# Kernel tuning notes

Measured on AMD Instinct MI355X. Metric: run time of the kernel, lower is better.

Reference implementation:

```python
import jax, jax.numpy as jnp
import numpy as np

N_SEQ, SEQ_LEN, BATCH, IN, H, OUT = 32, 256, 16, 32, 256, 1


def setup_inputs() -> dict:
    key = jax.random.key(0)
    ks = jax.random.split(key, 12)
    s = 1.0 / np.sqrt(H)  # torch RNNCell default init scale
    f32 = jnp.float32
    return {
        "x": jax.random.normal(ks[0], (N_SEQ, SEQ_LEN, BATCH, IN), f32),
        "flags": jax.random.randint(ks[1], (N_SEQ,), 0, 2, dtype=jnp.int32),
        "W_ih1": jax.random.normal(ks[2], (2, 4 * H, IN), f32) * s,
        "W_hh1": jax.random.normal(ks[3], (2, 4 * H, H), f32) * s,
        "b_ih1": jax.random.normal(ks[4], (2, 4 * H), f32) * s,
        "b_hh1": jax.random.normal(ks[5], (2, 4 * H), f32) * s,
        "W_ih2": jax.random.normal(ks[6], (4 * H, H), f32) * s,
        "W_hh2": jax.random.normal(ks[7], (4 * H, H), f32) * s,
        "b_ih2": jax.random.normal(ks[8], (4 * H,), f32) * s,
        "b_hh2": jax.random.normal(ks[9], (4 * H,), f32) * s,
        "W_lin": jax.random.normal(ks[10], (OUT, H), f32) * s,
        "b_lin": jax.random.normal(ks[11], (OUT,), f32) * s,
    }


def _lstm_cell(xt, h, c, Wih, Whh, b):
    # torch LSTMCell: gates = x@Wih.T + h@Whh.T + b_ih + b_hh; chunks i,f,g,o
    gates = xt @ Wih.T + h @ Whh.T + b
    i, f, g, o = jnp.split(gates, 4, axis=-1)
    c = jax.nn.sigmoid(f) * c + jax.nn.sigmoid(i) * jnp.tanh(g)
    h = jax.nn.sigmoid(o) * jnp.tanh(c)
    return h, c


def reference(x, flags, W_ih1, W_hh1, b_ih1, b_hh1,
              W_ih2, W_hh2, b_ih2, b_hh2, W_lin, b_lin):
    # flags selects layer1 (on-paper, idx 0) vs layer1_air (idx 1) per sequence
    Wih_s = W_ih1[flags]              # [N_SEQ, 4H, IN]
    Whh_s = W_hh1[flags]              # [N_SEQ, 4H, H]
    b_s = (b_ih1 + b_hh1)[flags]      # [N_SEQ, 4H]

    h0 = jnp.zeros((BATCH, H), x.dtype)

    def run_seq(xs, Wih, Whh, b):
        # hidden resets to zero at the start of every sequence -> independent scans
        def step(carry, xt):
            h, c = _lstm_cell(xt, *carry, Wih, Whh, b)
            return (h, c), None
        (h, _), _ = jax.lax.scan(step, (h0, h0), xs)
        return h

    h1 = jax.vmap(run_seq)(x, Wih_s, Whh_s, b_s)  # [N_SEQ, BATCH, H]

    # layer2: sequential LSTM over per-sequence final hiddens (dropout=0 -> identity)
    b2 = b_ih2 + b_hh2

    def step2(carry, hin):
        h, c = _lstm_cell(hin, *carry, W_ih2, W_hh2, b2)
        return (h, c), None

    (h2, _), _ = jax.lax.scan(step2, (h0, h0), h1)
    return jax.nn.sigmoid(h2 @ W_lin.T + b_lin)  # [BATCH, OUT]
```

## Files before the change

### kernel.cpp

```cpp
#include <hip/hip_runtime.h>
#include <hip/hip_bf16.h>

#define NSEQ   32
#define SEQLEN 256
#define NB     16
#define NIN    32
#define NH     256
#define G4     1024

typedef __attribute__((ext_vector_type(8))) short bf16x8;
typedef __attribute__((ext_vector_type(4))) float f32x4;
typedef unsigned long long ull;

__device__ __forceinline__ unsigned short f2bf(float f) {
    union { float f; unsigned u; } v; v.f = f;
    unsigned u = v.u;
    return (unsigned short)((u + 0x7FFFu + ((u >> 16) & 1u)) >> 16);
}
__device__ __forceinline__ float bf2f(unsigned short u) {
    union { unsigned u; float f; } v; v.u = ((unsigned)u) << 16; return v.f;
}
__device__ __forceinline__ float sigf(float x) { return 1.0f / (1.0f + __expf(-x)); }
__device__ __forceinline__ float tanhfast(float x) { return 1.0f - 2.0f / (__expf(2.0f * x) + 1.0f); }

__global__ void pack_w1(const float* __restrict__ Wih, const float* __restrict__ Whh,
                        unsigned short* __restrict__ Bp) {
    int idx = blockIdx.x * blockDim.x + threadIdx.x;
    if (idx >= 2 * 64 * 9 * 64) return;
    int fl   = idx / (64 * 9 * 64);
    int rem  = idx % (64 * 9 * 64);
    int tile = rem / (9 * 64);
    int kk   = (rem / 64) % 9;
    int l    = rem & 63;
    int n    = tile * 16 + (l & 15);
    int k0   = kk * 32 + (l >> 4) * 8;
    unsigned short* dst = Bp + (size_t)idx * 8;
#pragma unroll
    for (int j = 0; j < 8; ++j) {
        int k = k0 + j;
        float v = (k < NH) ? Whh[((size_t)fl * G4 + n) * NH + k]
                           : Wih[((size_t)fl * G4 + n) * NIN + (k - NH)];
        dst[j] = f2bf(v);
    }
}

__global__ void pack_w2(const float* __restrict__ Wih, const float* __restrict__ Whh,
                        unsigned short* __restrict__ Bp) {
    int idx = blockIdx.x * blockDim.x + threadIdx.x;
    if (idx >= 64 * 16 * 64) return;
    int tile = idx / (16 * 64);
    int kk   = (idx / 64) % 16;
    int l    = idx & 63;
    int n    = tile * 16 + (l & 15);
    int k0   = kk * 32 + (l >> 4) * 8;
    unsigned short* dst = Bp + (size_t)idx * 8;
#pragma unroll
    for (int j = 0; j < 8; ++j) {
        int k = k0 + j;
        float v = (k < NH) ? Whh[(size_t)n * NH + k] : Wih[(size_t)n * NH + (k - NH)];
        dst[j] = f2bf(v);
    }
}

#define STRA 320
#define ASH_BYTES (NB * STRA * 2)

__device__ __forceinline__ unsigned aoff(int row, int col) {
    return (((unsigned)(row * STRA + col)) * 2u) ^ (((unsigned)row & 7u) << 4);
}

__global__ __launch_bounds__(1024) void lstm_layer1(
    const float* __restrict__ x, const int* __restrict__ flags,
    const float* __restrict__ bih, const float* __restrict__ bhh,
    const unsigned short* __restrict__ Bp_all,
    unsigned short* __restrict__ h1bf,
    unsigned* __restrict__ hxu)
{
    __shared__ __align__(16) unsigned char Ash[ASH_BYTES];
    __shared__ float gate[4][64][17];

    const int bid = blockIdx.x;
    const int s   = bid & 31;
    const int j   = bid >> 5;
    const int tid = threadIdx.x;
    const int w = tid >> 6, l = tid & 63, lr = l & 15, kg = l >> 4;
    const int g = w >> 2, cg = w & 3;
    const int fl = flags[s];
    const int tile = g * 16 + j * 4 + cg;
    const unsigned short* Bp = Bp_all + (size_t)fl * (64 * 9 * 64 * 8);

    bf16x8 wreg[9];
#pragma unroll
    for (int kk = 0; kk < 9; ++kk)
        wreg[kk] = *(const bf16x8*)(Bp + ((size_t)(tile * 9 + kk) * 64 + l) * 8);

    const int grow = tile * 16 + lr;
    const float bias = bih[fl * G4 + grow] + bhh[fl * G4 + grow];

    const int pb = tid >> 6, pc = tid & 63;
    const int o0 = (((j + 1) & 3) << 6) + pc;
    const int o1 = (((j + 2) & 3) << 6) + pc;
    const int o2 = (((j + 3) & 3) << 6) + pc;
    const int xb = tid >> 5, xk = tid & 31;
    float cst = 0.f;

    unsigned* hxseq = hxu + (size_t)s * (2 * NB * 256);

    for (int i = tid * 4; i < ASH_BYTES; i += 1024 * 4)
        *(unsigned*)(Ash + i) = 0u;
    __syncthreads();
    if (tid < NB * NIN)
        *(unsigned short*)(Ash + aoff(xb, NH + xk)) =
            f2bf(x[(((size_t)s * SEQLEN) * NB + xb) * NIN + xk]);
    __syncthreads();

    for (int t = 0; t < SEQLEN; ++t) {
        float xpre = 0.f;
        if (t + 1 < SEQLEN && tid < NB * NIN)
            xpre = x[(((size_t)s * SEQLEN + t + 1) * NB + xb) * NIN + xk];

        f32x4 acc = {bias, bias, bias, bias};
#pragma unroll
        for (int kk = 0; kk < 9; ++kk) {
            bf16x8 a = *(const bf16x8*)(Ash + aoff(lr, kk * 32 + kg * 8));
            acc = __builtin_amdgcn_mfma_f32_16x16x32_bf16(a, wreg[kk], acc, 0, 0, 0);
        }
#pragma unroll
        for (int r = 0; r < 4; ++r)
            gate[g][cg * 16 + lr][kg * 4 + r] = acc[r];
        __syncthreads();

        float ig = gate[0][pc][pb], fg = gate[1][pc][pb];
        float gg = gate[2][pc][pb], og = gate[3][pc][pb];
        float cn = sigf(fg) * cst + sigf(ig) * tanhfast(gg);
        cst = cn;
        float h = sigf(og) * tanhfast(cn);
        unsigned short hb = f2bf(h);
        *(unsigned short*)(Ash + aoff(pb, (j << 6) + pc)) = hb;

        if (t == SEQLEN - 1) {
            h1bf[((size_t)s * NB + pb) * NH + (j << 6) + pc] = hb;
        } else {
            const unsigned tg = (unsigned)(t + 1);
            unsigned* row = hxseq + ((((t + 1) & 1) * NB + pb) << 8);
            __hip_atomic_store(row + (j << 6) + pc, ((unsigned)hb << 16) | tg,
                               __ATOMIC_RELAXED, __HIP_MEMORY_SCOPE_AGENT);
            if (tid < NB * NIN)
                *(unsigned short*)(Ash + aoff(xb, NH + xk)) = f2bf(xpre);
            unsigned v0 = __hip_atomic_load(row + o0, __ATOMIC_RELAXED, __HIP_MEMORY_SCOPE_AGENT);
            unsigned v1 = __hip_atomic_load(row + o1, __ATOMIC_RELAXED, __HIP_MEMORY_SCOPE_AGENT);
            unsigned v2 = __hip_atomic_load(row + o2, __ATOMIC_RELAXED, __HIP_MEMORY_SCOPE_AGENT);
            while ((v0 & 0xFFFFu) != tg)
                v0 = __hip_atomic_load(row + o0, __ATOMIC_RELAXED, __HIP_MEMORY_SCOPE_AGENT);
            while ((v1 & 0xFFFFu) != tg)
                v1 = __hip_atomic_load(row + o1, __ATOMIC_RELAXED, __HIP_MEMORY_SCOPE_AGENT);
            while ((v2 & 0xFFFFu) != tg)
                v2 = __hip_atomic_load(row + o2, __ATOMIC_RELAXED, __HIP_MEMORY_SCOPE_AGENT);
            *(unsigned short*)(Ash + aoff(pb, o0)) = (unsigned short)(v0 >> 16);
            *(unsigned short*)(Ash + aoff(pb, o1)) = (unsigned short)(v1 >> 16);
            *(unsigned short*)(Ash + aoff(pb, o2)) = (unsigned short)(v2 >> 16);
            __syncthreads();
        }
    }
}

#define STRA2 520

__global__ __launch_bounds__(1024, 4) void lstm_layer2(
    const unsigned short* __restrict__ h1bf,
    const float* __restrict__ bih2, const float* __restrict__ bhh2,
    const unsigned short* __restrict__ Bp2,
    const float* __restrict__ Wlin, const float* __restrict__ blin,
    float* __restrict__ out,
    ull* __restrict__ hx2)
{
    const int j = blockIdx.x;

    __shared__ __align__(16) unsigned short A_sh[NB * STRA2];
    __shared__ float gate[4][64][17];
    __shared__ float red[NB * 16];

    const int tid = threadIdx.x;
    const int w = tid >> 6, l = tid & 63, lr = l & 15, kg = l >> 4;
    const int g = w >> 2, cg = w & 3;
    const int tile = g * 16 + j * 4 + cg;

    bf16x8 wreg[16];
#pragma unroll
    for (int kk = 0; kk < 16; ++kk)
        wreg[kk] = *(const bf16x8*)(Bp2 + ((size_t)(tile * 16 + kk) * 64 + l) * 8);

    const int grow = tile * 16 + lr;
    const float bias = bih2[grow] + bhh2[grow];
    const int pb = tid >> 6, pc = tid & 63;
    float cst = 0.f;
    const int rb = tid >> 6, rc4 = (tid & 63) * 4;

    for (int i = tid; i < NB * NH; i += 1024)
        A_sh[(i >> 8) * STRA2 + (i & 255)] = 0;
    *(ushort4*)&A_sh[rb * STRA2 + NH + rc4] = *(const ushort4*)&h1bf[(size_t)rb * NH + rc4];
    __syncthreads();

    for (int sq = 0; sq < NSEQ; ++sq) {
        ushort4 pre = {0, 0, 0, 0};
        if (sq + 1 < NSEQ)
            pre = *(const ushort4*)&h1bf[((size_t)(sq + 1) * NB + rb) * NH + rc4];

        f32x4 acc = {bias, bias, bias, bias};
#pragma unroll
        for (int kk = 0; kk < 16; ++kk) {
            bf16x8 a = *(const bf16x8*)&A_sh[lr * STRA2 + kk * 32 + kg * 8];
            acc = __builtin_amdgcn_mfma_f32_16x16x32_bf16(a, wreg[kk], acc, 0, 0, 0);
        }
#pragma unroll
        for (int r = 0; r < 4; ++r)
            gate[g][cg * 16 + lr][kg * 4 + r] = acc[r];
        __syncthreads();

        {
            float ig = gate[0][pc][pb], fg = gate[1][pc][pb];
            float gg = gate[2][pc][pb], og = gate[3][pc][pb];
            float cn = sigf(fg) * cst + sigf(ig) * tanhfast(gg);
            cst = cn;
            float h = sigf(og) * tanhfast(cn);
            unsigned hw = ((unsigned)f2bf(h) << 16) | (unsigned)(sq + 1);
            A_sh[pb * STRA2 + (j << 6) + pc] = (unsigned short)(hw >> 16);
            __hip_atomic_store((unsigned*)hx2 + ((((sq + 1) & 1) * NB + pb) << 8) + (j << 6) + pc,
                               hw, __ATOMIC_RELAXED, __HIP_MEMORY_SCOPE_AGENT);
        }
        if (sq + 1 < NSEQ)
            *(ushort4*)&A_sh[rb * STRA2 + NH + rc4] = pre;

        {
            const unsigned tg = (unsigned)(sq + 1);
            unsigned* row = (unsigned*)hx2 + ((((sq + 1) & 1) * NB + pb) << 8);
            const int q0 = (((j + 1) & 3) << 6) + pc;
            const int q1 = (((j + 2) & 3) << 6) + pc;
            const int q2 = (((j + 3) & 3) << 6) + pc;
            unsigned v0 = __hip_atomic_load(row + q0, __ATOMIC_RELAXED, __HIP_MEMORY_SCOPE_AGENT);
            unsigned v1 = __hip_atomic_load(row + q1, __ATOMIC_RELAXED, __HIP_MEMORY_SCOPE_AGENT);
            unsigned v2 = __hip_atomic_load(row + q2, __ATOMIC_RELAXED, __HIP_MEMORY_SCOPE_AGENT);
            while ((v0 & 0xFFFFu) != tg)
                v0 = __hip_atomic_load(row + q0, __ATOMIC_RELAXED, __HIP_MEMORY_SCOPE_AGENT);
            while ((v1 & 0xFFFFu) != tg)
                v1 = __hip_atomic_load(row + q1, __ATOMIC_RELAXED, __HIP_MEMORY_SCOPE_AGENT);
            while ((v2 & 0xFFFFu) != tg)
                v2 = __hip_atomic_load(row + q2, __ATOMIC_RELAXED, __HIP_MEMORY_SCOPE_AGENT);
            A_sh[pb * STRA2 + q0] = (unsigned short)(v0 >> 16);
            A_sh[pb * STRA2 + q1] = (unsigned short)(v1 >> 16);
            A_sh[pb * STRA2 + q2] = (unsigned short)(v2 >> 16);
        }
        __syncthreads();
    }

    if (j == 0) {
        if (tid < 256) {
            int b = tid >> 4, kc = tid & 15;
            float pacc = 0.f;
#pragma unroll
            for (int k = 0; k < 16; ++k)
                pacc += bf2f(A_sh[b * STRA2 + kc * 16 + k]) * Wlin[kc * 16 + k];
            red[b * 16 + kc] = pacc;
        }
        __syncthreads();
        if (tid < 16) {
            float ssum = blin[0];
#pragma unroll
            for (int kc = 0; kc < 16; ++kc) ssum += red[tid * 16 + kc];
            out[tid] = 1.0f / (1.0f + __expf(-ssum));
        }
    }
}

extern "C" void kernel_launch(void* const* d_in, const int* in_sizes, int n_in,
                              void* d_out, int out_size, void* d_ws, size_t ws_size,
                              hipStream_t stream) {
    const float* x    = (const float*)d_in[0];
    const int*   flg  = (const int*)d_in[1];
    const float* Wih1 = (const float*)d_in[2];
    const float* Whh1 = (const float*)d_in[3];
    const float* bih1 = (const float*)d_in[4];
    const float* bhh1 = (const float*)d_in[5];
    const float* Wih2 = (const float*)d_in[6];
    const float* Whh2 = (const float*)d_in[7];
    const float* bih2 = (const float*)d_in[8];
    const float* bhh2 = (const float*)d_in[9];
    const float* Wlin = (const float*)d_in[10];
    const float* blin = (const float*)d_in[11];
    float* out = (float*)d_out;

    unsigned short* ws   = (unsigned short*)d_ws;
    unsigned short* Bp1  = ws;
    unsigned short* Bp2  = Bp1 + 589824;
    unsigned short* h1bf = Bp2 + 524288;
    unsigned*       hxu1 = (unsigned*)(h1bf + 131072);
    ull*            hx2  = (ull*)(hxu1 + 262144);

    hipMemsetAsync(hxu1, 0, 262144 * 4 + 4096 * 8, stream);

    pack_w1<<<dim3(288), dim3(256), 0, stream>>>(Wih1, Whh1, Bp1);
    pack_w2<<<dim3(256), dim3(256), 0, stream>>>(Wih2, Whh2, Bp2);
    lstm_layer1<<<dim3(128), dim3(1024), 0, stream>>>(x, flg, bih1, bhh1, Bp1, h1bf, hxu1);
    lstm_layer2<<<dim3(4), dim3(1024), 0, stream>>>(h1bf, bih2, bhh2, Bp2, Wlin, blin, out, hx2);
}
```

Before: 677.2 us.

## Add fast-path plain-load polling with atomic fallback and split MFMA accumulators

Each step writes its hidden-state word to two exchange buffers: a plain-store fast buffer and the existing agent-scope atomic buffer. Peers first poll the fast buffer with volatile loads under a budget and drop permanently to the atomic path if that ever times out. The aim is to cut cross-block handoff latency in the recurrent loop, relying on the hardware making plain stores visible to other CUs. The MFMA chains are also split across two accumulators to shorten the dependency chain. Layer2 now launches 32 blocks with only every eighth one active, apparently to spread the four working blocks across different XCDs.

Result: faster. 625.9 us (-7.6%).

```diff
diff --git a/kernel.cpp b/kernel.cpp
--- a/kernel.cpp
+++ b/kernel.cpp
@@ -74,7 +74,8 @@
     const float* __restrict__ bih, const float* __restrict__ bhh,
     const unsigned short* __restrict__ Bp_all,
     unsigned short* __restrict__ h1bf,
-    unsigned* __restrict__ hxu)
+    unsigned* __restrict__ hxS,
+    unsigned* __restrict__ hxF)
 {
     __shared__ __align__(16) unsigned char Ash[ASH_BYTES];
     __shared__ float gate[4][64][17];
@@ -103,8 +104,10 @@
     const int o2 = (((j + 3) & 3) << 6) + pc;
     const int xb = tid >> 5, xk = tid & 31;
     float cst = 0.f;
-
-    unsigned* hxseq = hxu + (size_t)s * (2 * NB * 256);
+    int mode = 0;
+
+    unsigned* hxSs = hxS + (size_t)s * (2 * NB * 256);
+    unsigned* hxFs = hxF + (size_t)s * (2 * NB * 256);
 
     for (int i = tid * 4; i < ASH_BYTES; i += 1024 * 4)
         *(unsigned*)(Ash + i) = 0u;
@@ -120,14 +123,20 @@
             xpre = x[(((size_t)s * SEQLEN + t + 1) * NB + xb) * NIN + xk];
 
         f32x4 acc = {bias, bias, bias, bias};
-#pragma unroll
-        for (int kk = 0; kk < 9; ++kk) {
+        f32x4 accB = {0.f, 0.f, 0.f, 0.f};
+#pragma unroll
+        for (int kk = 0; kk < 5; ++kk) {
             bf16x8 a = *(const bf16x8*)(Ash + aoff(lr, kk * 32 + kg * 8));
             acc = __builtin_amdgcn_mfma_f32_16x16x32_bf16(a, wreg[kk], acc, 0, 0, 0);
         }
 #pragma unroll
+        for (int kk = 5; kk < 9; ++kk) {
+            bf16x8 a = *(const bf16x8*)(Ash + aoff(lr, kk * 32 + kg * 8));
+            accB = __builtin_amdgcn_mfma_f32_16x16x32_bf16(a, wreg[kk], accB, 0, 0, 0);
+        }
+#pragma unroll
         for (int r = 0; r < 4; ++r)
-            gate[g][cg * 16 + lr][kg * 4 + r] = acc[r];
+            gate[g][cg * 16 + lr][kg * 4 + r] = acc[r] + accB[r];
         __syncthreads();
 
         float ig = gate[0][pc][pb], fg = gate[1][pc][pb];
@@ -142,20 +151,39 @@
             h1bf[((size_t)s * NB + pb) * NH + (j << 6) + pc] = hb;
         } else {
             const unsigned tg = (unsigned)(t + 1);
-            unsigned* row = hxseq + ((((t + 1) & 1) * NB + pb) << 8);
-            __hip_atomic_store(row + (j << 6) + pc, ((unsigned)hb << 16) | tg,
+            const unsigned word = ((unsigned)hb << 16) | tg;
+            const size_t ro = (size_t)((((t + 1) & 1) * NB + pb) << 8);
+            unsigned* rowF = hxFs + ro;
+            unsigned* rowS = hxSs + ro;
+            rowF[(j << 6) + pc] = word;
+            __hip_atomic_store(rowS + (j << 6) + pc, word,
                                __ATOMIC_RELAXED, __HIP_MEMORY_SCOPE_AGENT);
             if (tid < NB * NIN)
                 *(unsigned short*)(Ash + aoff(xb, NH + xk)) = f2bf(xpre);
-            unsigned v0 = __hip_atomic_load(row + o0, __ATOMIC_RELAXED, __HIP_MEMORY_SCOPE_AGENT);
-            unsigned v1 = __hip_atomic_load(row + o1, __ATOMIC_RELAXED, __HIP_MEMORY_SCOPE_AGENT);
-            unsigned v2 = __hip_atomic_load(row + o2, __ATOMIC_RELAXED, __HIP_MEMORY_SCOPE_AGENT);
-            while ((v0 & 0xFFFFu) != tg)
-                v0 = __hip_atomic_load(row + o0, __ATOMIC_RELAXED, __HIP_MEMORY_SCOPE_AGENT);
-            while ((v1 & 0xFFFFu) != tg)
-                v1 = __hip_atomic_load(row + o1, __ATOMIC_RELAXED, __HIP_MEMORY_SCOPE_AGENT);
-            while ((v2 & 0xFFFFu) != tg)
-                v2 = __hip_atomic_load(row + o2, __ATOMIC_RELAXED, __HIP_MEMORY_SCOPE_AGENT);
+
+            unsigned v0, v1, v2;
+            bool ok = false;
+            if (mode != 2) {
+                int budget = (mode == 0) ? 256 : 4000;
+                volatile const unsigned* F = rowF;
+                v0 = F[o0]; v1 = F[o1]; v2 = F[o2];
+                while ((v0 & 0xFFFFu) != tg && budget-- > 0) v0 = F[o0];
+                while ((v1 & 0xFFFFu) != tg && budget-- > 0) v1 = F[o1];
+                while ((v2 & 0xFFFFu) != tg && budget-- > 0) v2 = F[o2];
+                ok = ((v0 & 0xFFFFu) == tg) && ((v1 & 0xFFFFu) == tg) && ((v2 & 0xFFFFu) == tg);
+                mode = ok ? 1 : 2;
+            }
+            if (!ok) {
+                v0 = __hip_atomic_load(rowS + o0, __ATOMIC_RELAXED, __HIP_MEMORY_SCOPE_AGENT);
+                v1 = __hip_atomic_load(rowS + o1, __ATOMIC_RELAXED, __HIP_MEMORY_SCOPE_AGENT);
+                v2 = __hip_atomic_load(rowS + o2, __ATOMIC_RELAXED, __HIP_MEMORY_SCOPE_AGENT);
+                while ((v0 & 0xFFFFu) != tg)
+                    v0 = __hip_atomic_load(rowS + o0, __ATOMIC_RELAXED, __HIP_MEMORY_SCOPE_AGENT);
+                while ((v1 & 0xFFFFu) != tg)
+                    v1 = __hip_atomic_load(rowS + o1, __ATOMIC_RELAXED, __HIP_MEMORY_SCOPE_AGENT);
+                while ((v2 & 0xFFFFu) != tg)
+                    v2 = __hip_atomic_load(rowS + o2, __ATOMIC_RELAXED, __HIP_MEMORY_SCOPE_AGENT);
+            }
             *(unsigned short*)(Ash + aoff(pb, o0)) = (unsigned short)(v0 >> 16);
             *(unsigned short*)(Ash + aoff(pb, o1)) = (unsigned short)(v1 >> 16);
             *(unsigned short*)(Ash + aoff(pb, o2)) = (unsigned short)(v2 >> 16);
@@ -166,15 +194,18 @@
 
 #define STRA2 520
 
-__global__ __launch_bounds__(1024, 4) void lstm_layer2(
+__global__ __launch_bounds__(1024) void lstm_layer2(
     const unsigned short* __restrict__ h1bf,
     const float* __restrict__ bih2, const float* __restrict__ bhh2,
     const unsigned short* __restrict__ Bp2,
     const float* __restrict__ Wlin, const float* __restrict__ blin,
     float* __restrict__ out,
-    ull* __restrict__ hx2)
+    unsigned* __restrict__ hx2S,
+    unsigned* __restrict__ hx2F)
 {
-    const int j = blockIdx.x;
+    const int bid = blockIdx.x;
+    if (bid & 7) return;
+    const int j = bid >> 3;
 
     __shared__ __align__(16) unsigned short A_sh[NB * STRA2];
     __shared__ float gate[4][64][17];
@@ -194,7 +225,11 @@
     const float bias = bih2[grow] + bhh2[grow];
     const int pb = tid >> 6, pc = tid & 63;
     float cst = 0.f;
+    int mode = 0;
     const int rb = tid >> 6, rc4 = (tid & 63) * 4;
+    const int q0 = (((j + 1) & 3) << 6) + pc;
+    const int q1 = (((j + 2) & 3) << 6) + pc;
+    const int q2 = (((j + 3) & 3) << 6) + pc;
 
     for (int i = tid; i < NB * NH; i += 1024)
         A_sh[(i >> 8) * STRA2 + (i & 255)] = 0;
@@ -207,45 +242,65 @@
             pre = *(const ushort4*)&h1bf[((size_t)(sq + 1) * NB + rb) * NH + rc4];
 
         f32x4 acc = {bias, bias, bias, bias};
-#pragma unroll
-        for (int kk = 0; kk < 16; ++kk) {
+        f32x4 accB = {0.f, 0.f, 0.f, 0.f};
+#pragma unroll
+        for (int kk = 0; kk < 8; ++kk) {
             bf16x8 a = *(const bf16x8*)&A_sh[lr * STRA2 + kk * 32 + kg * 8];
             acc = __builtin_amdgcn_mfma_f32_16x16x32_bf16(a, wreg[kk], acc, 0, 0, 0);
         }
 #pragma unroll
+        for (int kk = 8; kk < 16; ++kk) {
+            bf16x8 a = *(const bf16x8*)&A_sh[lr * STRA2 + kk * 32 + kg * 8];
+            accB = __builtin_amdgcn_mfma_f32_16x16x32_bf16(a, wreg[kk], accB, 0, 0, 0);
+        }
+#pragma unroll
         for (int r = 0; r < 4; ++r)
-            gate[g][cg * 16 + lr][kg * 4 + r] = acc[r];
+            gate[g][cg * 16 + lr][kg * 4 + r] = acc[r] + accB[r];
         __syncthreads();
 
+        const unsigned tg = (unsigned)(sq + 1);
+        const size_t ro = (size_t)((((sq + 1) & 1) * NB + pb) << 8);
+        unsigned* rowF = hx2F + ro;
+        unsigned* rowS = hx2S + ro;
         {
             float ig = gate[0][pc][pb], fg = gate[1][pc][pb];
             float gg = gate[2][pc][pb], og = gate[3][pc][pb];
             float cn = sigf(fg) * cst + sigf(ig) * tanhfast(gg);
             cst = cn;
             float h = sigf(og) * tanhfast(cn);
-            unsigned hw = ((unsigned)f2bf(h) << 16) | (unsigned)(sq + 1);
-            A_sh[pb * STRA2 + (j << 6) + pc] = (unsigned short)(hw >> 16);
-            __hip_atomic_store((unsigned*)hx2 + ((((sq + 1) & 1) * NB + pb) << 8) + (j << 6) + pc,
-                               hw, __ATOMIC_RELAXED, __HIP_MEMORY_SCOPE_AGENT);
+            unsigned word = ((unsigned)f2bf(h) << 16) | tg;
+            A_sh[pb * STRA2 + (j << 6) + pc] = (unsigned short)(word >> 16);
+            rowF[(j << 6) + pc] = word;
+            __hip_atomic_store(rowS + (j << 6) + pc, word,
+                               __ATOMIC_RELAXED, __HIP_MEMORY_SCOPE_AGENT);
         }
         if (sq + 1 < NSEQ)
             *(ushort4*)&A_sh[rb * STRA2 + NH + rc4] = pre;
 
         {
-            const unsigned tg = (unsigned)(sq + 1);
-            unsigned* row = (unsigned*)hx2 + ((((sq + 1) & 1) * NB + pb) << 8);
-            const int q0 = (((j + 1) & 3) << 6) + pc;
-            const int q1 = (((j + 2) & 3) << 6) + pc;
-            const int q2 = (((j + 3) & 3) << 6) + pc;
-            unsigned v0 = __hip_atomic_load(row + q0, __ATOMIC_RELAXED, __HIP_MEMORY_SCOPE_AGENT);
-            unsigned v1 = __hip_atomic_load(row + q1, __ATOMIC_RELAXED, __HIP_MEMORY_SCOPE_AGENT);
-            unsigned v2 = __hip_atomic_load(row + q2, __ATOMIC_RELAXED, __HIP_MEMORY_SCOPE_AGENT);
-            while ((v0 & 0xFFFFu) != tg)
-                v0 = __hip_atomic_load(row + q0, __ATOMIC_RELAXED, __HIP_MEMORY_SCOPE_AGENT);
-            while ((v1 & 0xFFFFu) != tg)
-                v1 = __hip_atomic_load(row + q1, __ATOMIC_RELAXED, __HIP_MEMORY_SCOPE_AGENT);
-            while ((v2 & 0xFFFFu) != tg)
-                v2 = __hip_atomic_load(row + q2, __ATOMIC_RELAXED, __HIP_MEMORY_SCOPE_AGENT);
+            unsigned v0, v1, v2;
+            bool ok = false;
+            if (mode != 2) {
+                int budget = (mode == 0) ? 256 : 4000;
+                volatile const unsigned* F = rowF;
+                v0 = F[q0]; v1 = F[q1]; v2 = F[q2];
+                while ((v0 & 0xFFFFu) != tg && budget-- > 0) v0 = F[q0];
+                while ((v1 & 0xFFFFu) != tg && budget-- > 0) v1 = F[q1];
+                while ((v2 & 0xFFFFu) != tg && budget-- > 0) v2 = F[q2];
+                ok = ((v0 & 0xFFFFu) == tg) && ((v1 & 0xFFFFu) == tg) && ((v2 & 0xFFFFu) == tg);
+                mode = ok ? 1 : 2;
+            }
+            if (!ok) {
+                v0 = __hip_atomic_load(rowS + q0, __ATOMIC_RELAXED, __HIP_MEMORY_SCOPE_AGENT);
+                v1 = __hip_atomic_load(rowS + q1, __ATOMIC_RELAXED, __HIP_MEMORY_SCOPE_AGENT);
+                v2 = __hip_atomic_load(rowS + q2, __ATOMIC_RELAXED, __HIP_MEMORY_SCOPE_AGENT);
+                while ((v0 & 0xFFFFu) != tg)
+                    v0 = __hip_atomic_load(rowS + q0, __ATOMIC_RELAXED, __HIP_MEMORY_SCOPE_AGENT);
+                while ((v1 & 0xFFFFu) != tg)
+                    v1 = __hip_atomic_load(rowS + q1, __ATOMIC_RELAXED, __HIP_MEMORY_SCOPE_AGENT);
+                while ((v2 & 0xFFFFu) != tg)
+                    v2 = __hip_atomic_load(rowS + q2, __ATOMIC_RELAXED, __HIP_MEMORY_SCOPE_AGENT);
+            }
             A_sh[pb * STRA2 + q0] = (unsigned short)(v0 >> 16);
             A_sh[pb * STRA2 + q1] = (unsigned short)(v1 >> 16);
             A_sh[pb * STRA2 + q2] = (unsigned short)(v2 >> 16);
@@ -293,13 +348,15 @@
     unsigned short* Bp1  = ws;
     unsigned short* Bp2  = Bp1 + 589824;
     unsigned short* h1bf = Bp2 + 524288;
-    unsigned*       hxu1 = (unsigned*)(h1bf + 131072);
-    ull*            hx2  = (ull*)(hxu1 + 262144);
-
-    hipMemsetAsync(hxu1, 0, 262144 * 4 + 4096 * 8, stream);
+    unsigned*       hxS1 = (unsigned*)(h1bf + 131072);
+    unsigned*       hxF1 = hxS1 + 262144;
+    unsigned*       hx2S = hxF1 + 262144;
+    unsigned*       hx2F = hx2S + 8192;
+
+    hipMemsetAsync(hxS1, 0, (size_t)(262144 * 2 + 8192 * 2) * 4, stream);
 
     pack_w1<<<dim3(288), dim3(256), 0, stream>>>(Wih1, Whh1, Bp1);
     pack_w2<<<dim3(256), dim3(256), 0, stream>>>(Wih2, Whh2, Bp2);
-    lstm_layer1<<<dim3(128), dim3(1024), 0, stream>>>(x, flg, bih1, bhh1, Bp1, h1bf, hxu1);
-    lstm_layer2<<<dim3(4), dim3(1024), 0, stream>>>(h1bf, bih2, bhh2, Bp2, Wlin, blin, out, hx2);
-}
+    lstm_layer1<<<dim3(128), dim3(1024), 0, stream>>>(x, flg, bih1, bhh1, Bp1, h1bf, hxS1, hxF1);
+    lstm_layer2<<<dim3(32), dim3(1024), 0, stream>>>(h1bf, bih2, bhh2, Bp2, Wlin, blin, out, hx2S, hx2F);
+}
```
